# Performance work log

Measured on AMD Instinct MI355X. Metric: run time of the kernel, lower is better.

Reference implementation:

```python
import jax, jax.numpy as jnp
import numpy as np

N = 50000      # nodes
E = 800000     # edges (avg degree 16)
C = 32         # channels per irrep
NE = 4         # chemical elements
L = 2          # num_interactions
NB = 8         # num Bessel radial basis fns
RCUT = 5.0
PPOW = 6       # polynomial cutoff power
SQRT3 = 1.7320508075688772
INV_SQRT3 = 1.0 / SQRT3
INV_SQRT2 = 0.7071067811865476


def _poly_cutoff(x):
    # MACE polynomial cutoff envelope, p = PPOW
    p = float(PPOW)
    f = (1.0 - (p + 1.0) * (p + 2.0) / 2.0 * x ** PPOW
         + p * (p + 2.0) * x ** (PPOW + 1)
         - p * (p + 1.0) / 2.0 * x ** (PPOW + 2))
    return f * (x < 1.0)


def setup_inputs() -> dict:
    ks = jax.random.split(jax.random.key(0), 12)
    positions = 3.0 * jax.random.normal(ks[0], (N, 3), jnp.float32)
    node_species = jax.random.randint(ks[1], (N,), 0, NE)
    edge_index = jax.random.randint(ks[2], (2, E), 0, N)

    def rn(k, shape, fan):
        return jax.random.normal(k, shape, jnp.float32) / np.sqrt(fan).astype(np.float32)

    return {
        "positions": positions,
        "node_species": node_species,
        "edge_index": edge_index,
        "w_embed": rn(ks[3], (NE, C), NE),
        "w_up": rn(ks[4], (L, 2, C, C), C),
        "mlp_w1": rn(ks[5], (L, NB, 64), NB),
        "mlp_w2": rn(ks[6], (L, 64, 64), 64),
        "mlp_w3": rn(ks[7], (L, 64, 5 * C), 64),
        "w_lin": rn(ks[8], (L, 2, C, C), C),
        "w_prod": 0.5 * rn(ks[9], (L, NE, C, 5), 1),
        "w_out": rn(ks[10], (L, 2, C, C), C),
    }


def reference(positions, node_species, edge_index, w_embed, w_up,
              mlp_w1, mlp_w2, mlp_w3, w_lin, w_prod, w_out):
    send, recv = edge_index[0], edge_index[1]

    # edge vectors, lengths, spherical harmonics (lmax=1, component norm)
    vec = positions[recv] - positions[send]                       # [E,3]
    length = jnp.linalg.norm(vec, axis=-1, keepdims=True)         # [E,1]
    unit = vec / (length + 1e-9)
    y1 = SQRT3 * unit                                             # [E,3] l=1 SH; l=0 SH == 1

    # Bessel radial embedding * polynomial cutoff
    n = jnp.arange(1, NB + 1, dtype=positions.dtype)
    rb = jnp.sqrt(2.0 / RCUT) * jnp.sin(n * jnp.pi * length / RCUT) / (length + 1e-9)  # [E,NB]
    edge_feats = rb * _poly_cutoff(length / RCUT)                 # [E,NB]

    # node embedding: one-hot(species) @ w_embed == table lookup
    f0 = w_embed[node_species]                                    # [N,C] scalars
    f1 = jnp.zeros((f0.shape[0], C, 3), f0.dtype)                 # [N,C,3] vectors

    for i in range(L):
        # linear_up (per-l channel mixing)
        f0 = f0 @ w_up[i, 0]
        f1 = jnp.einsum('ncx,cd->ndx', f1, w_up[i, 1])

        # conv_tp_weights MLP: per-edge weights for 5 CG paths x C channels
        h = jax.nn.silu(edge_feats @ mlp_w1[i])
        h = jax.nn.silu(h @ mlp_w2[i])
        w = (h @ mlp_w3[i]).reshape(-1, 5, C)                     # [E,5,C]

        # gather sender features; channelwise CG tensor product with edge SH
        x0, x1 = f0[send], f1[send]                               # [E,C], [E,C,3]
        dot = jnp.einsum('ecx,ex->ec', x1, y1)                    # 1x1->0 path
        m0 = w[:, 0] * x0 + w[:, 3] * dot * INV_SQRT3             # [E,C]
        cross = jnp.cross(x1, y1[:, None, :])                     # 1x1->1 path
        m1 = (w[:, 1][..., None] * x0[..., None] * y1[:, None, :]
              + w[:, 2][..., None] * x1
              + w[:, 4][..., None] * cross * INV_SQRT2)           # [E,C,3]

        # scatter_sum into receivers
        M0 = jax.ops.segment_sum(m0, recv, num_segments=f0.shape[0])
        M1 = jax.ops.segment_sum(m1, recv, num_segments=f0.shape[0])

        # interaction linear (per-l)
        f0 = M0 @ w_lin[i, 0]
        f1 = jnp.einsum('ncx,cd->ndx', M1, w_lin[i, 1])

        # element-dependent symmetric product basis (correlation 2)
        wp = w_prod[i][node_species]                              # [N,C,5]
        o0 = wp[..., 0] * f0 + wp[..., 1] * f0 * f0 + wp[..., 2] * jnp.sum(f1 * f1, -1)
        o1 = wp[..., 3][..., None] * f1 + wp[..., 4][..., None] * f0[..., None] * f1

        # product-layer linear (per-l)
        f0 = o0 @ w_out[i, 0]
        f1 = jnp.einsum('ncx,cd->ndx', o1, w_out[i, 1])

    return jnp.concatenate([f0[..., None], f1], axis=-1)          # [N,C,4]
```

## Files before the change

kernel.cpp:

```cpp
#include <hip/hip_runtime.h>
#include <hip/hip_bf16.h>

#define NN 50000
#define NEDG 800000
#define CH 32
#define NBF 8
#define ECAP 240000
#define NBLK ((NN + 1023) / 1024)

typedef _Float16 half2_t __attribute__((ext_vector_type(2)));
typedef _Float16 half4_t __attribute__((ext_vector_type(4)));
typedef _Float16 half8_t __attribute__((ext_vector_type(8)));
typedef float    f32x4   __attribute__((ext_vector_type(4)));

constexpr float RCUT_F = 5.0f;
constexpr float SQRT3_F = 1.7320508075688772f;
constexpr float INV_SQRT3_F = 0.57735026918962576f;
constexpr float INV_SQRT2_F = 0.70710678118654752f;
constexpr float PI_F = 3.14159265358979323846f;

__device__ __forceinline__ float silu_f(float x) { return x / (1.0f + __expf(-x)); }

__global__ void k_prep_geo(const float* __restrict__ pos, const int* __restrict__ ei,
                           int* __restrict__ hist, int* __restrict__ gcnt,
                           int* __restrict__ esend, int* __restrict__ erecv,
                           float* __restrict__ egeo)
{
    __shared__ int s_woff[4];
    __shared__ int s_base;
    const int tid = threadIdx.x;
    const int e = blockIdx.x * 256 + tid;
    const int lane = tid & 63, wid = tid >> 6;

    int s = ei[e], r = ei[NEDG + e];
    float dx = pos[r*3+0] - pos[s*3+0];
    float dy = pos[r*3+1] - pos[s*3+1];
    float dz = pos[r*3+2] - pos[s*3+2];
    float len = sqrtf(dx*dx + dy*dy + dz*dz);
    bool valid = (len > 0.0f && len < RCUT_F);

    unsigned long long bal = __ballot(valid);
    int wrank = __popcll(bal & ((1ull << lane) - 1ull));
    if (lane == 0) s_woff[wid] = __popcll(bal);
    __syncthreads();
    if (tid == 0) {
        int c0 = s_woff[0], c1 = s_woff[1], c2 = s_woff[2], c3 = s_woff[3];
        s_base = atomicAdd(gcnt, c0 + c1 + c2 + c3);
        s_woff[0] = 0; s_woff[1] = c0; s_woff[2] = c0 + c1; s_woff[3] = c0 + c1 + c2;
    }
    __syncthreads();
    if (!valid) return;
    atomicAdd(&hist[r], 1);
    int slot = s_base + s_woff[wid] + wrank;
    if (slot >= ECAP) return;
    esend[slot] = s; erecv[slot] = r;

    float inv = 1.0f / (len + 1e-9f);
    float x = len * (1.0f / RCUT_F);
    float x2 = x*x, x3 = x2*x;
    float x6 = x3*x3;
    float cut = 1.0f - 28.0f*x6 + 48.0f*x6*x - 21.0f*x6*x2;
    float pref = 0.632455532033675866f * inv * cut;
    float* gg = egeo + (size_t)slot * 12;
    gg[0] = SQRT3_F * dx * inv;
    gg[1] = SQRT3_F * dy * inv;
    gg[2] = SQRT3_F * dz * inv;
    gg[3] = 0.f;
    float arg = PI_F * len * (1.0f / RCUT_F);
    float sa, ca;
    __sincosf(arg, &sa, &ca);
    float c2 = 2.0f * ca;
    float sk0 = 0.f, sk1 = sa;
    gg[4] = pref * sk1;
    #pragma unroll
    for (int k = 1; k < NBF; ++k) {
        float sk = c2*sk1 - sk0;
        gg[4+k] = pref * sk;
        sk0 = sk1; sk1 = sk;
    }
}

__global__ void k_scan_block(const int* __restrict__ hist, int* __restrict__ rowtmp,
                             int* __restrict__ bsum)
{
    __shared__ int s_ws[16];
    int t = threadIdx.x, b = blockIdx.x;
    int i = b*1024 + t;
    int v = (i < NN) ? hist[i] : 0;
    int x = v;
    #pragma unroll
    for (int d = 1; d < 64; d <<= 1) { int o = __shfl_up(x, d); if ((t & 63) >= d) x += o; }
    if ((t & 63) == 63) s_ws[t >> 6] = x;
    __syncthreads();
    if (t < 16) {
        int w = s_ws[t];
        #pragma unroll
        for (int d = 1; d < 16; d <<= 1) { int o = __shfl_up(w, d); if (t >= d) w += o; }
        s_ws[t] = w;
    }
    __syncthreads();
    int woff = (t >= 64) ? s_ws[(t >> 6) - 1] : 0;
    if (i < NN) rowtmp[i] = woff + x - v;
    if (t == 1023) bsum[b] = s_ws[15];
}

__global__ void k_scan_top(const int* __restrict__ bsum, int* __restrict__ btop,
                           int* __restrict__ rowptrNN)
{
    int t = threadIdx.x;
    int v = (t < NBLK) ? bsum[t] : 0;
    int x = v;
    #pragma unroll
    for (int d = 1; d < 64; d <<= 1) { int o = __shfl_up(x, d); if (t >= d) x += o; }
    if (t < NBLK) btop[t] = x - v;
    if (t == NBLK - 1) *rowptrNN = x;
}

__global__ void k_scan_add(const int* __restrict__ rowtmp, const int* __restrict__ btop,
                           int* __restrict__ rowptr, int* __restrict__ cursor)
{
    int t = threadIdx.x, b = blockIdx.x;
    int i = b*1024 + t;
    if (i >= NN) return;
    int r = rowtmp[i] + btop[b];
    rowptr[i] = r;
    cursor[i] = r;
}

__global__ void k_perm(const int* __restrict__ gcnt, const int* __restrict__ erecv,
                       int* __restrict__ cursor, int* __restrict__ ipos)
{
    int slot = blockIdx.x * 256 + threadIdx.x;
    if (slot >= *gcnt || slot >= ECAP) return;
    int idx = atomicAdd(&cursor[erecv[slot]], 1);
    ipos[slot] = (idx < ECAP) ? idx : 0;
}

__global__ void k_wcomb(const float* __restrict__ wout0, const float* __restrict__ wup1,
                        float* __restrict__ wc)
{
    int o = blockIdx.x * 256 + threadIdx.x;
    if (o >= 2048) return;
    int l = o >> 10, c = (o >> 5) & 31, d = o & 31;
    const float* A = wout0 + l*1024;
    const float* B = wup1 + l*1024;
    float acc = 0.f;
    #pragma unroll 8
    for (int k = 0; k < 32; ++k) acc += A[c*32 + k] * B[k*32 + d];
    wc[o] = acc;
}

__global__ void k_embed_up(const int* __restrict__ species, const float* __restrict__ wemb,
                           const float* __restrict__ wup0, float4* __restrict__ fu4)
{
    __shared__ float s_wu[1024];
    __shared__ float s_v[8][32];
    int tid = threadIdx.x;
    for (int t = tid; t < 1024; t += 256) s_wu[t] = wup0[t];
    __syncthreads();
    int lane = tid & 31, g = tid >> 5;
    int n = blockIdx.x * 8 + g;
    s_v[g][lane] = wemb[species[n]*CH + lane];
    float acc = 0.f;
    #pragma unroll
    for (int k = 0; k < 32; ++k) acc += s_v[g][k] * s_wu[k*32 + lane];
    fu4[(size_t)n*32 + lane] = make_float4(acc, 0.f, 0.f, 0.f);
}

__global__ __launch_bounds__(256, 2)
void k_edge(const float4* __restrict__ fu4,
            const float* __restrict__ w1g, const float* __restrict__ w2g,
            const float* __restrict__ w3g,
            const int* __restrict__ esend, const int* __restrict__ ipos,
            const float* __restrict__ egeo, const int* __restrict__ nactp,
            half4_t* __restrict__ emsgh)
{
    __shared__ __align__(16) _Float16 s_h1t[32][72];
    __shared__ __align__(16) _Float16 s_h2t[32][72];
    __shared__ __align__(16) _Float16 s_wgt[32][168];
    __shared__ __align__(16) float    s_geo[2][32][8];
    __shared__ __align__(16) float4   s_y1[2][32];

    const int tid = threadIdx.x;
    const int lane64 = tid & 63, wv = tid >> 6;
    const int lane = tid & 31, g = tid >> 5;

    const int et = wv >> 1;
    const int ob = (wv & 1) * 5;
    const int ob2 = (wv & 1) * 2;
    const int brow = 16*et + (lane64 & 15);
    const int qq = lane64 >> 4;
    const int q8 = 8 * qq;
    const int q4 = 4 * qq;
    const int colb = lane64 & 15;

    float w1r[8];
    #pragma unroll
    for (int k = 0; k < 8; ++k) w1r[k] = w1g[k*64 + lane64];

    half8_t w2r[4];
    #pragma unroll
    for (int j = 0; j < 2; ++j)
        #pragma unroll
        for (int ks = 0; ks < 2; ++ks) {
            half8_t a;
            #pragma unroll
            for (int i = 0; i < 8; ++i)
                a[i] = (_Float16)w2g[(32*ks + q8 + i)*64 + 16*(ob2+j) + colb];
            w2r[j*2+ks] = a;
        }
    half8_t w3r[10];
    #pragma unroll
    for (int ot = 0; ot < 5; ++ot)
        #pragma unroll
        for (int ks = 0; ks < 2; ++ks) {
            half8_t a;
            #pragma unroll
            for (int i = 0; i < 8; ++i)
                a[i] = (_Float16)w3g[(32*ks + q8 + i)*160 + 16*(ob+ot) + colb];
            w3r[ot*2+ks] = a;
        }

    const int nact = *nactp;
    const int nact1 = nact - 1;
    const int ntile = (nact + 31) >> 5;
    const int gstride = gridDim.x;
    const int stg_e = tid >> 3, stg_k = tid & 7;

    int t0 = blockIdx.x;
    int se[4], csr[4];
    if (t0 < ntile) {
        int ee = min(t0*32 + stg_e, nact1);
        s_geo[0][stg_e][stg_k] = egeo[(size_t)ee*12 + 4 + stg_k];
        if (tid < 32) {
            int e2 = min(t0*32 + tid, nact1);
            s_y1[0][tid] = *(const float4*)(egeo + (size_t)e2*12);
        }
        #pragma unroll
        for (int e = 0; e < 4; ++e) {
            int eic = min(t0*32 + g*4 + e, nact1);
            se[e] = esend[eic];
            csr[e] = ipos[eic];
        }
    }
    __syncthreads();

    int b = 0;
    for (int t = t0; t < ntile; t += gstride) {
        const int tn = t + gstride;
        const bool hn = tn < ntile;

        float rbv = 0.f; float4 y1v = make_float4(0.f,0.f,0.f,0.f);
        int nse[4], ncsr[4];
        if (hn) {
            int ee = min(tn*32 + stg_e, nact1);
            rbv = egeo[(size_t)ee*12 + 4 + stg_k];
            if (tid < 32) {
                int e2 = min(tn*32 + tid, nact1);
                y1v = *(const float4*)(egeo + (size_t)e2*12);
            }
            #pragma unroll
            for (int e = 0; e < 4; ++e) {
                int eic = min(tn*32 + g*4 + e, nact1);
                nse[e] = esend[eic];
                ncsr[e] = ipos[eic];
            }
        }

        const int ebase = t*32 + g*4;
        const int nv = nact - ebase;
        float y1x[4], y1y[4], y1z[4];
        float x0[4], xx[4], xy[4], xz[4];
        #pragma unroll
        for (int e = 0; e < 4; ++e) {
            float4 qv = fu4[(size_t)se[e]*32 + lane];
            x0[e] = qv.x; xx[e] = qv.y; xy[e] = qv.z; xz[e] = qv.w;
            float4 yv = s_y1[b][g*4 + e];
            y1x[e] = yv.x; y1y[e] = yv.y; y1z[e] = yv.z;
        }

        {
            const int eb = wv*8;
            #pragma unroll
            for (int e = 0; e < 8; ++e) {
                float4 r1 = *(const float4*)&s_geo[b][eb+e][0];
                float4 r2 = *(const float4*)&s_geo[b][eb+e][4];
                float a = r1.x*w1r[0] + r1.y*w1r[1] + r1.z*w1r[2] + r1.w*w1r[3]
                        + r2.x*w1r[4] + r2.y*w1r[5] + r2.z*w1r[6] + r2.w*w1r[7];
                s_h1t[eb+e][lane64] = (_Float16)silu_f(a);
            }
        }

        __syncthreads();

        {
            f32x4 acc2[2] = {};
            #pragma unroll
            for (int ks = 0; ks < 2; ++ks) {
                half8_t bf = *(const half8_t*)&s_h1t[brow][32*ks + q8];
                #pragma unroll
                for (int j = 0; j < 2; ++j)
                    acc2[j] = __builtin_amdgcn_mfma_f32_16x16x32_f16(w2r[j*2+ks], bf, acc2[j], 0, 0, 0);
            }
            #pragma unroll
            for (int j = 0; j < 2; ++j) {
                half4_t hv;
                hv[0] = (_Float16)silu_f(acc2[j][0]);
                hv[1] = (_Float16)silu_f(acc2[j][1]);
                hv[2] = (_Float16)silu_f(acc2[j][2]);
                hv[3] = (_Float16)silu_f(acc2[j][3]);
                *(half4_t*)&s_h2t[brow][16*(ob2+j) + q4] = hv;
            }
        }

        __syncthreads();

        {
            f32x4 acc[5] = {};
            #pragma unroll
            for (int ks = 0; ks < 2; ++ks) {
                half8_t bf = *(const half8_t*)&s_h2t[brow][32*ks + q8];
                #pragma unroll
                for (int ot = 0; ot < 5; ++ot)
                    acc[ot] = __builtin_amdgcn_mfma_f32_16x16x32_f16(w3r[ot*2+ks], bf, acc[ot], 0, 0, 0);
            }
            #pragma unroll
            for (int ot = 0; ot < 5; ++ot) {
                half4_t hv;
                hv[0] = (_Float16)acc[ot][0];
                hv[1] = (_Float16)acc[ot][1];
                hv[2] = (_Float16)acc[ot][2];
                hv[3] = (_Float16)acc[ot][3];
                *(half4_t*)&s_wgt[brow][16*(ob+ot) + q4] = hv;
            }
        }

        if (hn) {
            s_geo[b^1][stg_e][stg_k] = rbv;
            if (tid < 32) s_y1[b^1][tid] = y1v;
        }

        __syncthreads();

        #pragma unroll
        for (int e = 0; e < 4; ++e) {
            if (e < nv) {
                const int le = g*4 + e;
                float w0v = (float)s_wgt[le][lane];
                float w1v = (float)s_wgt[le][32 + lane];
                float w2v = (float)s_wgt[le][64 + lane];
                float w3v = (float)s_wgt[le][96 + lane];
                float w4v = (float)s_wgt[le][128 + lane];
                float dot = xx[e]*y1x[e] + xy[e]*y1y[e] + xz[e]*y1z[e];
                float m0 = w0v*x0[e] + w3v*dot*INV_SQRT3_F;
                float cx = xy[e]*y1z[e] - xz[e]*y1y[e];
                float cy = xz[e]*y1x[e] - xx[e]*y1z[e];
                float cz = xx[e]*y1y[e] - xy[e]*y1x[e];
                float a = w1v*x0[e];
                float m1x = a*y1x[e] + w2v*xx[e] + w4v*cx*INV_SQRT2_F;
                float m1y = a*y1y[e] + w2v*xy[e] + w4v*cy*INV_SQRT2_F;
                float m1z = a*y1z[e] + w2v*xz[e] + w4v*cz*INV_SQRT2_F;
                half4_t mv;
                mv[0] = (_Float16)m0; mv[1] = (_Float16)m1x;
                mv[2] = (_Float16)m1y; mv[3] = (_Float16)m1z;
                emsgh[(size_t)csr[e]*32 + lane] = mv;
            }
        }

        #pragma unroll
        for (int e = 0; e < 4; ++e) { se[e] = nse[e]; csr[e] = ncsr[e]; }
        b ^= 1;
    }
}

__global__ __launch_bounds__(256, 2)
void k_node_out(const half4_t* __restrict__ emsgh, const int* __restrict__ rowptr,
                const int* __restrict__ species,
                const float* __restrict__ wlin, const float* __restrict__ wprod,
                const float* __restrict__ w2nd, float4* __restrict__ out4)
{
    __shared__ __align__(16) _Float16 s_m[4][4][16][40];
    __shared__ float s_wp[640];

    const int tid = threadIdx.x;
    const int lane64 = tid & 63, wv = tid >> 6;
    const int col = lane64 & 15;
    const int qq = lane64 >> 4;
    const int q8 = 8*qq, q4 = 4*qq;
    const int hw = lane64 >> 5;
    const int ch32 = lane64 & 31;

    for (int t = tid; t < 640; t += 256) s_wp[t] = wprod[t];
    __syncthreads();

    half8_t a1[4], a2[4];
    #pragma unroll
    for (int l = 0; l < 2; ++l)
        #pragma unroll
        for (int ot = 0; ot < 2; ++ot) {
            half8_t x, y;
            #pragma unroll
            for (int i = 0; i < 8; ++i) {
                x[i] = (_Float16)wlin[l*1024 + (q8+i)*32 + 16*ot + col];
                y[i] = (_Float16)w2nd[l*1024 + (q8+i)*32 + 16*ot + col];
            }
            a1[l*2+ot] = x; a2[l*2+ot] = y;
        }

    const int nbase = blockIdx.x * 64 + wv * 16;

    for (int j = 0; j < 8; ++j) {
        int ln = hw*8 + j;
        int n = min(nbase + ln, NN-1);
        int es = rowptr[n], ee = rowptr[n+1];
        float m0 = 0.f, m1 = 0.f, m2 = 0.f, m3 = 0.f;
        for (int e = es; e < ee; ++e) {
            half4_t mv = emsgh[(size_t)e*32 + ch32];
            m0 += (float)mv[0]; m1 += (float)mv[1];
            m2 += (float)mv[2]; m3 += (float)mv[3];
        }
        s_m[wv][0][ln][ch32] = (_Float16)m0;
        s_m[wv][1][ln][ch32] = (_Float16)m1;
        s_m[wv][2][ln][ch32] = (_Float16)m2;
        s_m[wv][3][ln][ch32] = (_Float16)m3;
    }

    f32x4 f[4][2];
    {
        half8_t bf0 = *(const half8_t*)&s_m[wv][0][col][q8];
        half8_t bf1 = *(const half8_t*)&s_m[wv][1][col][q8];
        half8_t bf2 = *(const half8_t*)&s_m[wv][2][col][q8];
        half8_t bf3 = *(const half8_t*)&s_m[wv][3][col][q8];
        f32x4 z = {};
        #pragma unroll
        for (int ot = 0; ot < 2; ++ot) {
            f[0][ot] = __builtin_amdgcn_mfma_f32_16x16x32_f16(a1[0+ot], bf0, z, 0, 0, 0);
            f[1][ot] = __builtin_amdgcn_mfma_f32_16x16x32_f16(a1[2+ot], bf1, z, 0, 0, 0);
            f[2][ot] = __builtin_amdgcn_mfma_f32_16x16x32_f16(a1[2+ot], bf2, z, 0, 0, 0);
            f[3][ot] = __builtin_amdgcn_mfma_f32_16x16x32_f16(a1[2+ot], bf3, z, 0, 0, 0);
        }
    }

    const int n = min(nbase + col, NN-1);
    const int spb = species[n] * 160;
    #pragma unroll
    for (int ot = 0; ot < 2; ++ot) {
        half4_t o0v, o1xv, o1yv, o1zv;
        #pragma unroll
        for (int r = 0; r < 4; ++r) {
            int ch = 16*ot + q4 + r;
            const float* wp = &s_wp[spb + ch*5];
            float p0 = wp[0], p1 = wp[1], p2 = wp[2], p3 = wp[3], p4 = wp[4];
            float f0 = f[0][ot][r], f1x = f[1][ot][r], f1y = f[2][ot][r], f1z = f[3][ot][r];
            float o0 = p0*f0 + p1*f0*f0 + p2*(f1x*f1x + f1y*f1y + f1z*f1z);
            float s1 = p3 + p4*f0;
            o0v[r]  = (_Float16)o0;
            o1xv[r] = (_Float16)(s1*f1x);
            o1yv[r] = (_Float16)(s1*f1y);
            o1zv[r] = (_Float16)(s1*f1z);
        }
        *(half4_t*)&s_m[wv][0][col][16*ot + q4] = o0v;
        *(half4_t*)&s_m[wv][1][col][16*ot + q4] = o1xv;
        *(half4_t*)&s_m[wv][2][col][16*ot + q4] = o1yv;
        *(half4_t*)&s_m[wv][3][col][16*ot + q4] = o1zv;
    }

    f32x4 F[4][2];
    {
        half8_t bf0 = *(const half8_t*)&s_m[wv][0][col][q8];
        half8_t bf1 = *(const half8_t*)&s_m[wv][1][col][q8];
        half8_t bf2 = *(const half8_t*)&s_m[wv][2][col][q8];
        half8_t bf3 = *(const half8_t*)&s_m[wv][3][col][q8];
        f32x4 z = {};
        #pragma unroll
        for (int ot = 0; ot < 2; ++ot) {
            F[0][ot] = __builtin_amdgcn_mfma_f32_16x16x32_f16(a2[0+ot], bf0, z, 0, 0, 0);
            F[1][ot] = __builtin_amdgcn_mfma_f32_16x16x32_f16(a2[2+ot], bf1, z, 0, 0, 0);
            F[2][ot] = __builtin_amdgcn_mfma_f32_16x16x32_f16(a2[2+ot], bf2, z, 0, 0, 0);
            F[3][ot] = __builtin_amdgcn_mfma_f32_16x16x32_f16(a2[2+ot], bf3, z, 0, 0, 0);
        }
    }

    #pragma unroll
    for (int ot = 0; ot < 2; ++ot)
        #pragma unroll
        for (int r = 0; r < 4; ++r) {
            int ch = 16*ot + q4 + r;
            out4[(size_t)n*32 + ch] = make_float4(F[0][ot][r], F[1][ot][r],
                                                  F[2][ot][r], F[3][ot][r]);
        }
}

static inline size_t align256(size_t x) { return (x + 255) & ~(size_t)255; }

extern "C" void kernel_launch(void* const* d_in, const int* in_sizes, int n_in,
                              void* d_out, int out_size, void* d_ws, size_t ws_size,
                              hipStream_t stream)
{
    const float* pos   = (const float*)d_in[0];
    const int* species = (const int*)d_in[1];
    const int* ei      = (const int*)d_in[2];
    const float* wemb  = (const float*)d_in[3];
    const float* wup   = (const float*)d_in[4];
    const float* mw1   = (const float*)d_in[5];
    const float* mw2   = (const float*)d_in[6];
    const float* mw3   = (const float*)d_in[7];
    const float* wlin  = (const float*)d_in[8];
    const float* wprod = (const float*)d_in[9];
    const float* wout  = (const float*)d_in[10];

    char* ws = (char*)d_ws;
    size_t off = 0;
    int* hist   = (int*)(ws + off);   off = align256(off + (size_t)(NN+1)*4);
    int* rowtmp = (int*)(ws + off);   off = align256(off + (size_t)NN*4);
    int* rowptr = (int*)(ws + off);   off = align256(off + (size_t)(NN+1)*4);
    int* cursor = (int*)(ws + off);   off = align256(off + (size_t)NN*4);
    int* bsum   = (int*)(ws + off);   off = align256(off + (size_t)64*4);
    int* btop   = (int*)(ws + off);   off = align256(off + (size_t)64*4);
    int* esend  = (int*)(ws + off);   off = align256(off + (size_t)ECAP*4);
    int* erecv  = (int*)(ws + off);   off = align256(off + (size_t)ECAP*4);
    int* ipos   = (int*)(ws + off);   off = align256(off + (size_t)ECAP*4);
    float* wc   = (float*)(ws + off); off = align256(off + (size_t)2048*4);
    float* egeo = (float*)(ws + off); off = align256(off + (size_t)ECAP*12*4);
    float4* fu4 = (float4*)(ws + off); off = align256(off + (size_t)NN*128*4);
    half4_t* emsgh = (half4_t*)(ws + off); off = align256(off + (size_t)ECAP*32*8);

    int* gcnt = hist + NN;
    int* nactp = rowptr + NN;

    hipMemsetAsync(hist, 0, (size_t)(NN+1)*sizeof(int), stream);
    k_prep_geo<<<NEDG/256, 256, 0, stream>>>(pos, ei, hist, gcnt, esend, erecv, egeo);
    k_scan_block<<<NBLK, 1024, 0, stream>>>(hist, rowtmp, bsum);
    k_scan_top<<<1, 64, 0, stream>>>(bsum, btop, nactp);
    k_scan_add<<<NBLK, 1024, 0, stream>>>(rowtmp, btop, rowptr, cursor);
    k_perm<<<(ECAP + 255)/256, 256, 0, stream>>>(gcnt, erecv, cursor, ipos);
    k_wcomb<<<8, 256, 0, stream>>>(wout, wup + 2048, wc);
    k_embed_up<<<NN/8, 256, 0, stream>>>(species, wemb, wup, fu4);

    const int node_grid = (NN + 63) / 64;
    for (int i = 0; i < 2; ++i) {
        k_edge<<<2048, 256, 0, stream>>>(fu4, mw1 + i*512, mw2 + i*4096, mw3 + i*10240,
                                         esend, ipos, egeo, nactp, emsgh);
        k_node_out<<<node_grid, 256, 0, stream>>>(emsgh, rowptr, species,
                                                  wlin + i*2048, wprod + i*640,
                                                  (i == 0) ? wc : (wout + 2048),
                                                  (i == 0) ? fu4 : (float4*)d_out);
    }
}
```

Measured before the change: 266.7 us.

## Store node features in fp16 and prebuild MFMA weight fragments

```diff
diff --git a/kernel.cpp b/kernel.cpp
--- a/kernel.cpp
+++ b/kernel.cpp
@@ -150,8 +150,38 @@
     wc[o] = acc;
 }
 
+__global__ void k_wfrag(const float* __restrict__ mw2, const float* __restrict__ mw3,
+                        _Float16* __restrict__ wtab)
+{
+    int idx = blockIdx.x * 256 + threadIdx.x;
+    if (idx >= 3584) return;
+    int layer = idx / 1792;
+    int r = idx - layer * 1792;
+    int q8, col, ks, j;
+    _Float16* dst;
+    const float* src;
+    int ld;
+    if (r < 512) {
+        int frag = r >> 6, l = r & 63;
+        ks = frag & 1; j = frag >> 1;
+        q8 = 8*(l >> 4); col = l & 15;
+        src = mw2 + layer*4096; ld = 64;
+        dst = wtab + layer*14336 + frag*512 + l*8;
+    } else {
+        r -= 512;
+        int frag = r >> 6, l = r & 63;
+        ks = frag & 1; j = frag >> 1;
+        q8 = 8*(l >> 4); col = l & 15;
+        src = mw3 + layer*10240; ld = 160;
+        dst = wtab + layer*14336 + 4096 + frag*512 + l*8;
+    }
+    #pragma unroll
+    for (int i = 0; i < 8; ++i)
+        dst[i] = (_Float16)src[(32*ks + q8 + i)*ld + 16*j + col];
+}
+
 __global__ void k_embed_up(const int* __restrict__ species, const float* __restrict__ wemb,
-                           const float* __restrict__ wup0, float4* __restrict__ fu4)
+                           const float* __restrict__ wup0, half4_t* __restrict__ fuh)
 {
     __shared__ float s_wu[1024];
     __shared__ float s_v[8][32];
@@ -164,13 +194,13 @@
     float acc = 0.f;
     #pragma unroll
     for (int k = 0; k < 32; ++k) acc += s_v[g][k] * s_wu[k*32 + lane];
-    fu4[(size_t)n*32 + lane] = make_float4(acc, 0.f, 0.f, 0.f);
+    half4_t hv; hv[0] = (_Float16)acc; hv[1] = 0; hv[2] = 0; hv[3] = 0;
+    fuh[(size_t)n*32 + lane] = hv;
 }
 
 __global__ __launch_bounds__(256, 2)
-void k_edge(const float4* __restrict__ fu4,
-            const float* __restrict__ w1g, const float* __restrict__ w2g,
-            const float* __restrict__ w3g,
+void k_edge(const half4_t* __restrict__ fuh,
+            const float* __restrict__ w1g, const _Float16* __restrict__ wtab,
             const int* __restrict__ esend, const int* __restrict__ ipos,
             const float* __restrict__ egeo, const int* __restrict__ nactp,
             half4_t* __restrict__ emsgh)
@@ -192,7 +222,6 @@
     const int qq = lane64 >> 4;
     const int q8 = 8 * qq;
     const int q4 = 4 * qq;
-    const int colb = lane64 & 15;
 
     float w1r[8];
     #pragma unroll
@@ -202,24 +231,14 @@
     #pragma unroll
     for (int j = 0; j < 2; ++j)
         #pragma unroll
-        for (int ks = 0; ks < 2; ++ks) {
-            half8_t a;
-            #pragma unroll
-            for (int i = 0; i < 8; ++i)
-                a[i] = (_Float16)w2g[(32*ks + q8 + i)*64 + 16*(ob2+j) + colb];
-            w2r[j*2+ks] = a;
-        }
+        for (int ks = 0; ks < 2; ++ks)
+            w2r[j*2+ks] = *(const half8_t*)&wtab[((ob2+j)*2+ks)*512 + lane64*8];
     half8_t w3r[10];
     #pragma unroll
     for (int ot = 0; ot < 5; ++ot)
         #pragma unroll
-        for (int ks = 0; ks < 2; ++ks) {
-            half8_t a;
-            #pragma unroll
-            for (int i = 0; i < 8; ++i)
-                a[i] = (_Float16)w3g[(32*ks + q8 + i)*160 + 16*(ob+ot) + colb];
-            w3r[ot*2+ks] = a;
-        }
+        for (int ks = 0; ks < 2; ++ks)
+            w3r[ot*2+ks] = *(const half8_t*)&wtab[4096 + ((ob+ot)*2+ks)*512 + lane64*8];
 
     const int nact = *nactp;
     const int nact1 = nact - 1;
@@ -273,8 +292,9 @@
         float x0[4], xx[4], xy[4], xz[4];
         #pragma unroll
         for (int e = 0; e < 4; ++e) {
-            float4 qv = fu4[(size_t)se[e]*32 + lane];
-            x0[e] = qv.x; xx[e] = qv.y; xy[e] = qv.z; xz[e] = qv.w;
+            half4_t qv = fuh[(size_t)se[e]*32 + lane];
+            x0[e] = (float)qv[0]; xx[e] = (float)qv[1];
+            xy[e] = (float)qv[2]; xz[e] = (float)qv[3];
             float4 yv = s_y1[b][g*4 + e];
             y1x[e] = yv.x; y1y[e] = yv.y; y1z[e] = yv.z;
         }
@@ -377,7 +397,8 @@
 void k_node_out(const half4_t* __restrict__ emsgh, const int* __restrict__ rowptr,
                 const int* __restrict__ species,
                 const float* __restrict__ wlin, const float* __restrict__ wprod,
-                const float* __restrict__ w2nd, float4* __restrict__ out4)
+                const float* __restrict__ w2nd,
+                half4_t* __restrict__ fuh_out, float4* __restrict__ dout)
 {
     __shared__ __align__(16) _Float16 s_m[4][4][16][40];
     __shared__ float s_wp[640];
@@ -481,14 +502,27 @@
         }
     }
 
-    #pragma unroll
-    for (int ot = 0; ot < 2; ++ot)
-        #pragma unroll
-        for (int r = 0; r < 4; ++r) {
-            int ch = 16*ot + q4 + r;
-            out4[(size_t)n*32 + ch] = make_float4(F[0][ot][r], F[1][ot][r],
-                                                  F[2][ot][r], F[3][ot][r]);
-        }
+    if (dout) {
+        #pragma unroll
+        for (int ot = 0; ot < 2; ++ot)
+            #pragma unroll
+            for (int r = 0; r < 4; ++r) {
+                int ch = 16*ot + q4 + r;
+                dout[(size_t)n*32 + ch] = make_float4(F[0][ot][r], F[1][ot][r],
+                                                      F[2][ot][r], F[3][ot][r]);
+            }
+    } else {
+        #pragma unroll
+        for (int ot = 0; ot < 2; ++ot)
+            #pragma unroll
+            for (int r = 0; r < 4; ++r) {
+                int ch = 16*ot + q4 + r;
+                half4_t hv;
+                hv[0] = (_Float16)F[0][ot][r]; hv[1] = (_Float16)F[1][ot][r];
+                hv[2] = (_Float16)F[2][ot][r]; hv[3] = (_Float16)F[3][ot][r];
+                fuh_out[(size_t)n*32 + ch] = hv;
+            }
+    }
 }
 
 static inline size_t align256(size_t x) { return (x + 255) & ~(size_t)255; }
@@ -521,8 +555,9 @@
     int* erecv  = (int*)(ws + off);   off = align256(off + (size_t)ECAP*4);
     int* ipos   = (int*)(ws + off);   off = align256(off + (size_t)ECAP*4);
     float* wc   = (float*)(ws + off); off = align256(off + (size_t)2048*4);
+    _Float16* wtab = (_Float16*)(ws + off); off = align256(off + (size_t)28672*2);
     float* egeo = (float*)(ws + off); off = align256(off + (size_t)ECAP*12*4);
-    float4* fu4 = (float4*)(ws + off); off = align256(off + (size_t)NN*128*4);
+    half4_t* fuh = (half4_t*)(ws + off); off = align256(off + (size_t)NN*32*8);
     half4_t* emsgh = (half4_t*)(ws + off); off = align256(off + (size_t)ECAP*32*8);
 
     int* gcnt = hist + NN;
@@ -535,15 +570,16 @@
     k_scan_add<<<NBLK, 1024, 0, stream>>>(rowtmp, btop, rowptr, cursor);
     k_perm<<<(ECAP + 255)/256, 256, 0, stream>>>(gcnt, erecv, cursor, ipos);
     k_wcomb<<<8, 256, 0, stream>>>(wout, wup + 2048, wc);
-    k_embed_up<<<NN/8, 256, 0, stream>>>(species, wemb, wup, fu4);
+    k_wfrag<<<14, 256, 0, stream>>>(mw2, mw3, wtab);
+    k_embed_up<<<NN/8, 256, 0, stream>>>(species, wemb, wup, fuh);
 
     const int node_grid = (NN + 63) / 64;
     for (int i = 0; i < 2; ++i) {
-        k_edge<<<2048, 256, 0, stream>>>(fu4, mw1 + i*512, mw2 + i*4096, mw3 + i*10240,
+        k_edge<<<2048, 256, 0, stream>>>(fuh, mw1 + i*512, wtab + i*14336,
                                          esend, ipos, egeo, nactp, emsgh);
         k_node_out<<<node_grid, 256, 0, stream>>>(emsgh, rowptr, species,
                                                   wlin + i*2048, wprod + i*640,
                                                   (i == 0) ? wc : (wout + 2048),
-                                                  (i == 0) ? fu4 : (float4*)d_out);
-    }
-}
+                                                  fuh, (i == 1) ? (float4*)d_out : nullptr);
+    }
+}
```

Result: faster. 240.0 us (-10.0%).
